# Performance work log

Measured on AMD Instinct MI355X. Metric: run time of the kernel, lower is better.

Reference implementation:

```python
import jax, jax.numpy as jnp
import numpy as np

B, S, D, H = 4, 4096, 1024, 16
DH = D // H


def setup_inputs() -> dict:
    key = jax.random.key(0)
    ks = jax.random.split(key, 8)
    scale = 1.0 / np.sqrt(D)
    return {
        "q": jax.random.normal(ks[0], (B, S, D), jnp.float32),
        "k": jax.random.normal(ks[1], (B, S, D), jnp.float32),
        "v": jax.random.normal(ks[2], (B, S, D), jnp.float32),
        "mask": jax.random.uniform(ks[3], (H, H), jnp.float32),
        # torch nn.Linear weights, layout [out, in]; applied as x @ W.T
        "Wq": jax.random.normal(ks[4], (D, D), jnp.float32) * scale,
        "Wk": jax.random.normal(ks[5], (D, D), jnp.float32) * scale,
        "Wv": jax.random.normal(ks[6], (D, D), jnp.float32) * scale,
        "Wo": jax.random.normal(ks[7], (D, D), jnp.float32) * scale,
    }


def reference(q, k, v, mask, Wq, Wk, Wv, Wo):
    # projections (bias-free Linear): x @ W.T, then split to [B,S,H,DH]
    qh = (q @ Wq.T).reshape(B, S, H, DH)
    kh = (k @ Wk.T).reshape(B, S, H, DH)
    vh = (v @ Wv.T).reshape(B, S, H, DH)
    # Faithful to source: NO head/seq transpose, so attention is over the
    # head axis per token: score [B,S,H,H]
    score = jnp.einsum('bshd,bsgd->bshg', qh, kh) / np.sqrt(DH)
    score = score * mask  # multiplicative mask, broadcast [H,H]
    p = jax.nn.softmax(score, axis=-1)
    attn = jnp.einsum('bshg,bsgd->bshd', p, vh)  # [B,S,H,DH]
    out = attn.reshape(B, S, D) @ Wo.T
    return out
```

## Files before the change

kernel.cpp:

```cpp
#include <hip/hip_runtime.h>
#include <hip/hip_bf16.h>
#include <stdint.h>


namespace {
constexpr int kD  = 1024;
constexpr int kH  = 16;
constexpr int kDH = 64;
constexpr int kM  = 4 * 4096;
constexpr size_t PER = (size_t)kM * kD;
constexpr size_t WSZ = (size_t)kD * kD;

typedef __attribute__((ext_vector_type(4))) float f32x4;
typedef __attribute__((ext_vector_type(8))) short s16x8;

__device__ __forceinline__ unsigned short f2b(float f) {
  uint32_t x = __builtin_bit_cast(uint32_t, f);
  x += 0x7fffu + ((x >> 16) & 1u);
  return (unsigned short)(x >> 16);
}
__device__ __forceinline__ float b2f(unsigned short u) {
  return __builtin_bit_cast(float, (uint32_t)u << 16);
}

typedef __attribute__((address_space(3))) void as3_void;
typedef __attribute__((address_space(1))) void as1_void;
__device__ __forceinline__ void gload_lds16(const void* g, void* l) {
  __builtin_amdgcn_global_load_lds((const as1_void*)(uintptr_t)g,
                                   (as3_void*)(uint32_t)(uintptr_t)l, 16, 0, 0);
}

__global__ __launch_bounds__(256) void cvt_bf16(
    const float* __restrict__ q, const float* __restrict__ k, const float* __restrict__ v,
    const float* __restrict__ Wq, const float* __restrict__ Wk, const float* __restrict__ Wv,
    const float* __restrict__ Wo, unsigned short* __restrict__ out) {
  const size_t total8 = (3 * PER + 4 * WSZ) / 8;
  for (size_t i8 = (size_t)blockIdx.x * blockDim.x + threadIdx.x; i8 < total8;
       i8 += (size_t)gridDim.x * blockDim.x) {
    size_t i = i8 * 8;
    const float* s; size_t o;
    if (i < 3 * PER) {
      if (i < PER)            { s = q; o = i; }
      else if (i < 2 * PER)   { s = k; o = i - PER; }
      else                    { s = v; o = i - 2 * PER; }
    } else {
      size_t j = i - 3 * PER;
      if (j < WSZ)            { s = Wq; o = j; }
      else if (j < 2 * WSZ)   { s = Wk; o = j - WSZ; }
      else if (j < 3 * WSZ)   { s = Wv; o = j - 2 * WSZ; }
      else                    { s = Wo; o = j - 3 * WSZ; }
    }
    f32x4 f0 = ((const f32x4*)(s + o))[0];
    f32x4 f1 = ((const f32x4*)(s + o))[1];
    s16x8 r;
#pragma unroll
    for (int d = 0; d < 4; ++d) {
      r[d]     = (short)f2b(f0[d]);
      r[4 + d] = (short)f2b(f1[d]);
    }
    *(s16x8*)(out + i) = r;
  }
}

constexpr int BM2 = 256, BN2 = 256, BK2 = 64;
constexpr int KT2 = kD / BK2;

__device__ __forceinline__ void mfma16(f32x4 (&a)[2][4], s16x8 (&af)[2][2],
                                       s16x8 (&bw)[4][2]) {
  __builtin_amdgcn_s_setprio(1);
#pragma unroll
  for (int mi = 0; mi < 2; ++mi)
#pragma unroll
    for (int nj = 0; nj < 4; ++nj)
#pragma unroll
      for (int kk = 0; kk < 2; ++kk)
        a[mi][nj] = __builtin_amdgcn_mfma_f32_16x16x32_bf16(af[mi][kk], bw[nj][kk],
                                                            a[mi][nj], 0, 0, 0);
  __builtin_amdgcn_s_setprio(0);
}

template <bool OUT_F32>
__device__ __forceinline__ void gemmq_body(const unsigned short* __restrict__ A,
                                           const unsigned short* __restrict__ Bm,
                                           void* __restrict__ Cp) {
  constexpr int K = kD, N = kD;
  __shared__ __align__(16) unsigned short lds[65536];

  const int lin = blockIdx.y * gridDim.x + blockIdx.x;
  const int xcd = lin & 7;
  const int idx = lin >> 3;
  const int m0 = (xcd * 8 + (idx >> 2)) * BM2;
  const int n0 = (idx & 3) * BN2;

  const int t    = threadIdx.x;
  const int lane = t & 63;
  const int w    = t >> 6;
  const int wrow = w >> 1;
  const int wcol = w & 1;

  const int srow  = lane >> 3;
  const int sslot = (lane & 7) ^ srow;
  const int fr     = lane & 15;
  const int fkslot = lane >> 4;

  auto stageHalf = [&](const unsigned short* src, int grow0, int k0, int slot) {
    const unsigned short* g = src + (size_t)(grow0 + w * 16 + srow) * K + k0 + sslot * 8;
    unsigned short* l = lds + slot * 8192 + w * 16 * 64;
    gload_lds16(g, l);
    gload_lds16(g + (size_t)8 * K, l + 8 * 64);
  };
  auto rdA = [&](int slot, int mi, int kk) -> s16x8 {
    int r = wrow * 32 + mi * 16 + fr;
    int s16 = (kk * 4 + fkslot) ^ (r & 7);
    return *(const s16x8*)(lds + slot * 8192 + r * 64 + s16 * 8);
  };
  auto rdB = [&](int slot, int nj, int kk) -> s16x8 {
    int r = wcol * 64 + nj * 16 + fr;
    int s16 = (kk * 4 + fkslot) ^ (r & 7);
    return *(const s16x8*)(lds + slot * 8192 + r * 64 + s16 * 8);
  };

  f32x4 acc[4][2][4];
#pragma unroll
  for (int qi = 0; qi < 4; ++qi)
#pragma unroll
    for (int mi = 0; mi < 2; ++mi)
#pragma unroll
      for (int nj = 0; nj < 4; ++nj) acc[qi][mi][nj] = (f32x4){0.f, 0.f, 0.f, 0.f};

  stageHalf(A,  m0,       0, 0);
  stageHalf(Bm, n0,       0, 2);
  stageHalf(Bm, n0 + 128, 0, 3);
  stageHalf(A,  m0 + 128, 0, 1);
  stageHalf(A,  m0,       BK2, 4);
  stageHalf(Bm, n0 + 128, BK2, 7);
  asm volatile("s_waitcnt vmcnt(4)" ::: "memory");
  __builtin_amdgcn_s_barrier();

  s16x8 af[2][2], bw[4][2];

  for (int tt = 0; tt < KT2; ++tt) {
    const int b  = (tt & 1) * 4;
    const int nb = b ^ 4;
    const int k1 = (tt + 1) * BK2;
    const int k2 = (tt + 2) * BK2;

    if (tt + 1 < KT2) stageHalf(A, m0 + 128, k1, nb + 1);
#pragma unroll
    for (int mi = 0; mi < 2; ++mi)
#pragma unroll
      for (int kk = 0; kk < 2; ++kk) af[mi][kk] = rdA(b + 0, mi, kk);
#pragma unroll
    for (int nj = 0; nj < 4; ++nj)
#pragma unroll
      for (int kk = 0; kk < 2; ++kk) bw[nj][kk] = rdB(b + 2, nj, kk);
    __builtin_amdgcn_s_barrier();
    asm volatile("s_waitcnt lgkmcnt(0)" ::: "memory");
    __builtin_amdgcn_sched_barrier(0);
    mfma16(acc[0], af, bw);
    __builtin_amdgcn_s_barrier();

    if (tt + 1 < KT2) stageHalf(Bm, n0, k1, nb + 2);
#pragma unroll
    for (int nj = 0; nj < 4; ++nj)
#pragma unroll
      for (int kk = 0; kk < 2; ++kk) bw[nj][kk] = rdB(b + 3, nj, kk);
    __builtin_amdgcn_s_barrier();
    asm volatile("s_waitcnt lgkmcnt(0)" ::: "memory");
    __builtin_amdgcn_sched_barrier(0);
    mfma16(acc[1], af, bw);
    __builtin_amdgcn_s_barrier();

    if (tt + 2 < KT2) stageHalf(A, m0, k2, b + 0);
#pragma unroll
    for (int mi = 0; mi < 2; ++mi)
#pragma unroll
      for (int kk = 0; kk < 2; ++kk) af[mi][kk] = rdA(b + 1, mi, kk);
    __builtin_amdgcn_s_barrier();
    asm volatile("s_waitcnt lgkmcnt(0)" ::: "memory");
    __builtin_amdgcn_sched_barrier(0);
    mfma16(acc[2], af, bw);
    __builtin_amdgcn_s_barrier();

    if (tt + 2 < KT2) stageHalf(Bm, n0 + 128, k2, b + 3);
    if (tt <= KT2 - 3)      { asm volatile("s_waitcnt vmcnt(4)" ::: "memory"); }
    else if (tt == KT2 - 2) { asm volatile("s_waitcnt vmcnt(0)" ::: "memory"); }
#pragma unroll
    for (int nj = 0; nj < 4; ++nj)
#pragma unroll
      for (int kk = 0; kk < 2; ++kk) bw[nj][kk] = rdB(b + 2, nj, kk);
    __builtin_amdgcn_s_barrier();
    asm volatile("s_waitcnt lgkmcnt(0)" ::: "memory");
    __builtin_amdgcn_sched_barrier(0);
    mfma16(acc[3], af, bw);
    __builtin_amdgcn_s_barrier();
  }

  constexpr int MH[4] = {0, 0, 1, 1};
  constexpr int NH[4] = {0, 1, 1, 0};
  const int cr = (lane >> 4) * 4;
  const int cc = lane & 15;
#pragma unroll
  for (int qi = 0; qi < 4; ++qi)
#pragma unroll
    for (int mi = 0; mi < 2; ++mi)
#pragma unroll
      for (int nj = 0; nj < 4; ++nj)
#pragma unroll
        for (int r = 0; r < 4; ++r) {
          size_t row = (size_t)(m0 + MH[qi] * 128 + wrow * 32 + mi * 16 + cr + r);
          size_t col = (size_t)(n0 + NH[qi] * 128 + wcol * 64 + nj * 16 + cc);
          if constexpr (OUT_F32)
            ((float*)Cp)[row * N + col] = acc[qi][mi][nj][r];
          else
            ((unsigned short*)Cp)[row * N + col] = f2b(acc[qi][mi][nj][r]);
        }
}

__global__ __launch_bounds__(512, 2) void proj_gemmq(
    const unsigned short* __restrict__ qb, const unsigned short* __restrict__ kb,
    const unsigned short* __restrict__ vb, const unsigned short* __restrict__ Wqb,
    const unsigned short* __restrict__ Wkb, const unsigned short* __restrict__ Wvb,
    unsigned short* __restrict__ qh, unsigned short* __restrict__ kh,
    unsigned short* __restrict__ vh) {
  const unsigned short *A, *W;
  unsigned short* C;
  if (blockIdx.z == 0)      { A = qb; W = Wqb; C = qh; }
  else if (blockIdx.z == 1) { A = kb; W = Wkb; C = kh; }
  else                      { A = vb; W = Wvb; C = vh; }
  gemmq_body<false>(A, W, C);
}

__global__ __launch_bounds__(512, 2) void out_gemmq(const unsigned short* __restrict__ attn,
                                                    const unsigned short* __restrict__ Wob,
                                                    float* __restrict__ out) {
  gemmq_body<true>(attn, Wob, out);
}

__global__ __launch_bounds__(256) void attn_tok(const unsigned short* __restrict__ qh,
                                                const unsigned short* __restrict__ kh,
                                                const unsigned short* __restrict__ vh,
                                                const float* __restrict__ mask,
                                                unsigned short* __restrict__ attn) {
  __shared__ float P[4][16][17];
  __shared__ __align__(16) unsigned short Vs[4][16 * 64];
  const int lane = threadIdx.x & 63;
  const int wid  = threadIdx.x >> 6;
  const size_t tok = (size_t)blockIdx.x * 4 + wid;

  const unsigned short* qp = qh + tok * kD;
  const unsigned short* kp = kh + tok * kD;
  const unsigned short* vp = vh + tok * kD;

  {
    const s16x8* src = (const s16x8*)vp;
    s16x8 a = src[2 * lane], b = src[2 * lane + 1];
    s16x8* dst = (s16x8*)Vs[wid];
    dst[2 * lane] = a;
    dst[2 * lane + 1] = b;
  }

  const int fr = lane & 15;
  const int fk = (lane >> 4) * 8;
  s16x8 a0 = *(const s16x8*)(qp + fr * kDH + fk);
  s16x8 a1 = *(const s16x8*)(qp + fr * kDH + 32 + fk);
  s16x8 b0 = *(const s16x8*)(kp + fr * kDH + fk);
  s16x8 b1 = *(const s16x8*)(kp + fr * kDH + 32 + fk);
  f32x4 s = {0.f, 0.f, 0.f, 0.f};
  s = __builtin_amdgcn_mfma_f32_16x16x32_bf16(a0, b0, s, 0, 0, 0);
  s = __builtin_amdgcn_mfma_f32_16x16x32_bf16(a1, b1, s, 0, 0, 0);

  const int cr = (lane >> 4) * 4;
  const int cc = lane & 15;
  float p[4];
#pragma unroll
  for (int r = 0; r < 4; ++r) {
    float val = s[r] * 0.125f * mask[(cr + r) * kH + cc];
    float mx = val;
#pragma unroll
    for (int d = 1; d < 16; d <<= 1) mx = fmaxf(mx, __shfl_xor(mx, d));
    float e = __expf(val - mx);
    float sum = e;
#pragma unroll
    for (int d = 1; d < 16; d <<= 1) sum += __shfl_xor(sum, d);
    p[r] = e / sum;
  }
#pragma unroll
  for (int r = 0; r < 4; ++r) P[wid][cr + r][cc] = p[r];

  const int h  = lane >> 2;
  const int d0 = (lane & 3) * 16;
  float o[16];
#pragma unroll
  for (int i = 0; i < 16; ++i) o[i] = 0.f;
#pragma unroll
  for (int g = 0; g < 16; ++g) {
    float pg = P[wid][h][g];
    s16x8 v0 = *(const s16x8*)(Vs[wid] + g * kDH + d0);
    s16x8 v1 = *(const s16x8*)(Vs[wid] + g * kDH + d0 + 8);
#pragma unroll
    for (int dd = 0; dd < 8; ++dd) {
      o[dd]     += pg * b2f((unsigned short)v0[dd]);
      o[8 + dd] += pg * b2f((unsigned short)v1[dd]);
    }
  }
  unsigned short* op = attn + tok * kD + h * kDH + d0;
  s16x8 r0, r1;
#pragma unroll
  for (int dd = 0; dd < 8; ++dd) {
    r0[dd] = (short)f2b(o[dd]);
    r1[dd] = (short)f2b(o[dd + 8]);
  }
  *(s16x8*)op = r0;
  *(s16x8*)(op + 8) = r1;
}

constexpr int BM = 128, BN = 128, BK = 32;
constexpr int LDSP = BK + 8;
__device__ __forceinline__ void cvt16_store(const float* __restrict__ g, short* __restrict__ l) {
  const f32x4* s4 = (const f32x4*)g;
  f32x4 f0 = s4[0], f1 = s4[1], f2 = s4[2], f3 = s4[3];
  s16x8 o0, o1;
#pragma unroll
  for (int i = 0; i < 4; ++i) {
    o0[i]     = (short)f2b(f0[i]);
    o0[4 + i] = (short)f2b(f1[i]);
    o1[i]     = (short)f2b(f2[i]);
    o1[4 + i] = (short)f2b(f3[i]);
  }
  *(s16x8*)l = o0;
  *(s16x8*)(l + 8) = o1;
}

template <bool A_BF16, bool OUT_F32>
__device__ __forceinline__ void gemm_body_cvt(const void* __restrict__ Ap,
                                              const float* __restrict__ Wp,
                                              void* __restrict__ Cp) {
  constexpr int N = kD, K = kD;
  __shared__ short As[BM * LDSP];
  __shared__ short Bs[BN * LDSP];
  const int t  = threadIdx.x;
  const int m0 = blockIdx.y * BM;
  const int n0 = blockIdx.x * BN;
  const int srow = t >> 1;
  const int scol = (t & 1) * 16;
  const int lane = t & 63;
  const int wid  = t >> 6;
  const int wm   = (wid >> 1) * 64;
  const int wn   = (wid & 1) * 64;
  const int fr   = lane & 15;
  const int fk   = (lane >> 4) * 8;

  f32x4 acc[4][4];
#pragma unroll
  for (int i = 0; i < 4; ++i)
#pragma unroll
    for (int j = 0; j < 4; ++j) acc[i][j] = (f32x4){0.f, 0.f, 0.f, 0.f};

  for (int k0 = 0; k0 < K; k0 += BK) {
    if constexpr (A_BF16) {
      const unsigned short* Ab = (const unsigned short*)Ap;
      const s16x8* src = (const s16x8*)(Ab + (size_t)(m0 + srow) * K + k0 + scol);
      s16x8 v0 = src[0], v1 = src[1];
      *(s16x8*)(As + srow * LDSP + scol) = v0;
      *(s16x8*)(As + srow * LDSP + scol + 8) = v1;
    } else {
      cvt16_store((const float*)Ap + (size_t)(m0 + srow) * K + k0 + scol,
                  As + srow * LDSP + scol);
    }
    cvt16_store(Wp + (size_t)(n0 + srow) * K + k0 + scol, Bs + srow * LDSP + scol);
    __syncthreads();
    s16x8 af[4], bw[4];
#pragma unroll
    for (int i = 0; i < 4; ++i)
      af[i] = *(const s16x8*)(As + (wm + i * 16 + fr) * LDSP + fk);
#pragma unroll
    for (int j = 0; j < 4; ++j)
      bw[j] = *(const s16x8*)(Bs + (wn + j * 16 + fr) * LDSP + fk);
#pragma unroll
    for (int i = 0; i < 4; ++i)
#pragma unroll
      for (int j = 0; j < 4; ++j)
        acc[i][j] = __builtin_amdgcn_mfma_f32_16x16x32_bf16(af[i], bw[j], acc[i][j], 0, 0, 0);
    __syncthreads();
  }
  const int cr = (lane >> 4) * 4;
  const int cc = lane & 15;
#pragma unroll
  for (int i = 0; i < 4; ++i)
#pragma unroll
    for (int j = 0; j < 4; ++j)
#pragma unroll
      for (int r = 0; r < 4; ++r) {
        size_t row = (size_t)(m0 + wm + i * 16 + cr + r);
        size_t col = (size_t)(n0 + wn + j * 16 + cc);
        if constexpr (OUT_F32)
          ((float*)Cp)[row * N + col] = acc[i][j][r];
        else
          ((unsigned short*)Cp)[row * N + col] = f2b(acc[i][j][r]);
      }
}

__global__ __launch_bounds__(256) void proj_gemm_cvt(
    const float* __restrict__ q, const float* __restrict__ k, const float* __restrict__ v,
    const float* __restrict__ Wq, const float* __restrict__ Wk, const float* __restrict__ Wv,
    unsigned short* __restrict__ qh, unsigned short* __restrict__ kh,
    unsigned short* __restrict__ vh) {
  const float* A; const float* W; unsigned short* C;
  if (blockIdx.z == 0)      { A = q; W = Wq; C = qh; }
  else if (blockIdx.z == 1) { A = k; W = Wk; C = kh; }
  else                      { A = v; W = Wv; C = vh; }
  gemm_body_cvt<false, false>(A, W, C);
}

__global__ __launch_bounds__(256) void out_gemm_cvt(const unsigned short* __restrict__ attn,
                                                    const float* __restrict__ Wo,
                                                    float* __restrict__ out) {
  gemm_body_cvt<true, true>(attn, Wo, out);
}

}

extern "C" void kernel_launch(void* const* d_in, const int* in_sizes, int n_in,
                              void* d_out, int out_size, void* d_ws, size_t ws_size,
                              hipStream_t stream) {
  (void)in_sizes; (void)n_in; (void)out_size;
  const float* q    = (const float*)d_in[0];
  const float* k    = (const float*)d_in[1];
  const float* v    = (const float*)d_in[2];
  const float* mask = (const float*)d_in[3];
  const float* Wq   = (const float*)d_in[4];
  const float* Wk   = (const float*)d_in[5];
  const float* Wv   = (const float*)d_in[6];
  const float* Wo   = (const float*)d_in[7];

  const size_t need = (6 * PER + 4 * WSZ) * sizeof(unsigned short);
  if (ws_size >= need) {
    unsigned short* qb  = (unsigned short*)d_ws;
    unsigned short* kb  = qb + PER;
    unsigned short* vb  = kb + PER;
    unsigned short* Wqb = vb + PER;
    unsigned short* Wkb = Wqb + WSZ;
    unsigned short* Wvb = Wkb + WSZ;
    unsigned short* Wob = Wvb + WSZ;
    unsigned short* qh  = Wob + WSZ;
    unsigned short* kh  = qh + PER;
    unsigned short* vh  = kh + PER;
    unsigned short* at  = qb;

    cvt_bf16<<<2048, 256, 0, stream>>>(q, k, v, Wq, Wk, Wv, Wo, qb);
    proj_gemmq<<<dim3(kD / BN2, kM / BM2, 3), 512, 0, stream>>>(qb, kb, vb, Wqb, Wkb, Wvb,
                                                                qh, kh, vh);
    attn_tok<<<dim3(kM / 4), 256, 0, stream>>>(qh, kh, vh, mask, at);
    out_gemmq<<<dim3(kD / BN2, kM / BM2), 512, 0, stream>>>(at, Wob, (float*)d_out);
  } else {
    unsigned short* qh = (unsigned short*)d_ws;
    unsigned short* kh = qh + PER;
    unsigned short* vh = kh + PER;
    unsigned short* at = (ws_size >= 4 * PER * sizeof(unsigned short)) ? (vh + PER) : qh;
    proj_gemm_cvt<<<dim3(kD / BN, kM / BM, 3), 256, 0, stream>>>(q, k, v, Wq, Wk, Wv,
                                                                 qh, kh, vh);
    attn_tok<<<dim3(kM / 4), 256, 0, stream>>>(qh, kh, vh, mask, at);
    out_gemm_cvt<<<dim3(kD / BN, kM / BM), 256, 0, stream>>>(at, Wo, (float*)d_out);
  }
}
```

Measured before the change: 232.7 us.

## Software-pipeline LDS fragment reads with MFMA using double-buffered register fragments

Restructures the GEMM main loop so the LDS reads for the next quadrant are issued before the current quadrant's MFMAs. Partial lgkmcnt waits replace full drains, and the loop is unrolled by two so the A and B fragment registers ping-pong between two sets. This cuts barriers per iteration and is meant to hide LDS read latency behind matrix math. The cost is more VGPRs, which could reduce occupancy, plus a more delicate wait and barrier ordering.

```diff
diff --git a/kernel.cpp b/kernel.cpp
--- a/kernel.cpp
+++ b/kernel.cpp
@@ -137,63 +137,73 @@
   asm volatile("s_waitcnt vmcnt(4)" ::: "memory");
   __builtin_amdgcn_s_barrier();
 
-  s16x8 af[2][2], bw[4][2];
-
-  for (int tt = 0; tt < KT2; ++tt) {
+  s16x8 afA[2][2], afB[2][2], bwX[4][2], bwY[4][2];
+
+#pragma unroll
+  for (int mi = 0; mi < 2; ++mi)
+#pragma unroll
+    for (int kk = 0; kk < 2; ++kk) afA[mi][kk] = rdA(0, mi, kk);
+#pragma unroll
+  for (int nj = 0; nj < 4; ++nj)
+#pragma unroll
+    for (int kk = 0; kk < 2; ++kk) bwX[nj][kk] = rdB(2, nj, kk);
+
+  auto tileBody = [&](int tt, s16x8 (&bw0)[4][2], s16x8 (&bw1)[4][2]) {
     const int b  = (tt & 1) * 4;
     const int nb = b ^ 4;
     const int k1 = (tt + 1) * BK2;
     const int k2 = (tt + 2) * BK2;
 
+    __builtin_amdgcn_s_barrier();
+#pragma unroll
+    for (int nj = 0; nj < 4; ++nj)
+#pragma unroll
+      for (int kk = 0; kk < 2; ++kk) bw1[nj][kk] = rdB(b + 3, nj, kk);
     if (tt + 1 < KT2) stageHalf(A, m0 + 128, k1, nb + 1);
+    asm volatile("s_waitcnt lgkmcnt(8)" ::: "memory");
+    __builtin_amdgcn_sched_barrier(0);
+    mfma16(acc[0], afA, bw0);
+
+    __builtin_amdgcn_s_barrier();
 #pragma unroll
     for (int mi = 0; mi < 2; ++mi)
 #pragma unroll
-      for (int kk = 0; kk < 2; ++kk) af[mi][kk] = rdA(b + 0, mi, kk);
-#pragma unroll
-    for (int nj = 0; nj < 4; ++nj)
-#pragma unroll
-      for (int kk = 0; kk < 2; ++kk) bw[nj][kk] = rdB(b + 2, nj, kk);
+      for (int kk = 0; kk < 2; ++kk) afB[mi][kk] = rdA(b + 1, mi, kk);
+    if (tt + 1 < KT2) stageHalf(Bm, n0, k1, nb + 2);
+    asm volatile("s_waitcnt lgkmcnt(4)" ::: "memory");
+    __builtin_amdgcn_sched_barrier(0);
+    mfma16(acc[1], afA, bw1);
+
     __builtin_amdgcn_s_barrier();
+    if (tt + 2 < KT2) stageHalf(A, m0, k2, b + 0);
     asm volatile("s_waitcnt lgkmcnt(0)" ::: "memory");
     __builtin_amdgcn_sched_barrier(0);
-    mfma16(acc[0], af, bw);
+    mfma16(acc[2], afB, bw1);
+
+    if (tt + 1 < KT2) {
+      if (tt <= KT2 - 3) { asm volatile("s_waitcnt vmcnt(2)" ::: "memory"); }
+      else               { asm volatile("s_waitcnt vmcnt(0)" ::: "memory"); }
+    }
     __builtin_amdgcn_s_barrier();
-
-    if (tt + 1 < KT2) stageHalf(Bm, n0, k1, nb + 2);
-#pragma unroll
-    for (int nj = 0; nj < 4; ++nj)
-#pragma unroll
-      for (int kk = 0; kk < 2; ++kk) bw[nj][kk] = rdB(b + 3, nj, kk);
-    __builtin_amdgcn_s_barrier();
-    asm volatile("s_waitcnt lgkmcnt(0)" ::: "memory");
+    if (tt + 1 < KT2) {
+#pragma unroll
+      for (int mi = 0; mi < 2; ++mi)
+#pragma unroll
+        for (int kk = 0; kk < 2; ++kk) afA[mi][kk] = rdA(nb + 0, mi, kk);
+#pragma unroll
+      for (int nj = 0; nj < 4; ++nj)
+#pragma unroll
+        for (int kk = 0; kk < 2; ++kk) bw1[nj][kk] = rdB(nb + 2, nj, kk);
+      if (tt + 2 < KT2) stageHalf(Bm, n0 + 128, k2, b + 3);
+    }
     __builtin_amdgcn_sched_barrier(0);
-    mfma16(acc[1], af, bw);
-    __builtin_amdgcn_s_barrier();
-
-    if (tt + 2 < KT2) stageHalf(A, m0, k2, b + 0);
-#pragma unroll
-    for (int mi = 0; mi < 2; ++mi)
-#pragma unroll
-      for (int kk = 0; kk < 2; ++kk) af[mi][kk] = rdA(b + 1, mi, kk);
-    __builtin_amdgcn_s_barrier();
-    asm volatile("s_waitcnt lgkmcnt(0)" ::: "memory");
-    __builtin_amdgcn_sched_barrier(0);
-    mfma16(acc[2], af, bw);
-    __builtin_amdgcn_s_barrier();
-
-    if (tt + 2 < KT2) stageHalf(Bm, n0 + 128, k2, b + 3);
-    if (tt <= KT2 - 3)      { asm volatile("s_waitcnt vmcnt(4)" ::: "memory"); }
-    else if (tt == KT2 - 2) { asm volatile("s_waitcnt vmcnt(0)" ::: "memory"); }
-#pragma unroll
-    for (int nj = 0; nj < 4; ++nj)
-#pragma unroll
-      for (int kk = 0; kk < 2; ++kk) bw[nj][kk] = rdB(b + 2, nj, kk);
-    __builtin_amdgcn_s_barrier();
-    asm volatile("s_waitcnt lgkmcnt(0)" ::: "memory");
-    __builtin_amdgcn_sched_barrier(0);
-    mfma16(acc[3], af, bw);
-    __builtin_amdgcn_s_barrier();
+    mfma16(acc[3], afB, bw0);
+  };
+
+#pragma unroll
+  for (int it = 0; it < KT2 / 2; ++it) {
+    tileBody(2 * it,     bwX, bwY);
+    tileBody(2 * it + 1, bwY, bwX);
   }
 
   constexpr int MH[4] = {0, 0, 1, 1};
```

New measurement: 283.3 us. 1.22x slower.
